# Performance work log

Measured on AMD Instinct MI355X. Metric: run time of the kernel, lower is better.

The kernel has to match this reference:

```python
import jax, jax.numpy as jnp
import numpy as np

B, S, D = 1, 2048, 1024
NH, NKV, WS = 8, 2, 64
HD = D // NH  # 128
E, HDIM, TOPK = 16, 512, 2
FP16_MIN = -65504.0
EPS = 1e-6
AUX_COEFF = 1e-5


def rmsnorm(x, w):
    return x * jax.lax.rsqrt(jnp.mean(x * x, axis=-1, keepdims=True) + EPS) * w


def setup_inputs() -> dict:
    key = jax.random.key(0)
    ks = jax.random.split(key, 24)
    r = lambda k, shape, fan: jax.random.normal(k, shape, dtype=jnp.float32) * (1.0 / np.sqrt(fan))
    return {
        "x": jax.random.normal(ks[0], (B, S, D), dtype=jnp.float32),
        "norm1_w": jnp.ones((D,), jnp.float32),
        "wq": r(ks[1], (D, NH * HD), D), "bq": jnp.zeros((NH * HD,), jnp.float32),
        "wk": r(ks[2], (D, NKV * HD), D), "bk": jnp.zeros((NKV * HD,), jnp.float32),
        "wv": r(ks[3], (D, NKV * HD), D), "bv": jnp.zeros((NKV * HD,), jnp.float32),
        "wo": r(ks[4], (NH * HD, D), NH * HD), "bo": jnp.zeros((D,), jnp.float32),
        "sink_bias": jnp.zeros((), jnp.float32),
        "norm2_w": jnp.ones((D,), jnp.float32),
        "router_w": r(ks[5], (D, E), D), "router_b": jnp.zeros((E,), jnp.float32),
        "w1": r(ks[6], (E, D, HDIM), D), "b1": jnp.zeros((E, HDIM), jnp.float32),
        "w2": r(ks[7], (E, HDIM, D), HDIM), "b2": jnp.zeros((E, D), jnp.float32),
    }


def reference(x, norm1_w, wq, bq, wk, bk, wv, bv, wo, bo, sink_bias,
              norm2_w, router_w, router_b, w1, b1, w2, b2):
    # ---- sliding-window attention with sink softmax ----
    h = rmsnorm(x, norm1_w)
    q = (h @ wq + bq).reshape(B, S, NH, HD).transpose(0, 2, 1, 3)    # [B,NH,S,HD]
    k = (h @ wk + bk).reshape(B, S, NKV, HD).transpose(0, 2, 1, 3)   # [B,NKV,S,HD]
    v = (h @ wv + bv).reshape(B, S, NKV, HD).transpose(0, 2, 1, 3)
    k = jnp.repeat(k, NH // NKV, axis=1)  # GQA expand -> [B,NH,S,HD]
    v = jnp.repeat(v, NH // NKV, axis=1)
    scores = jnp.einsum('bhqd,bhkd->bhqk', q, k) / np.sqrt(HD)
    i = jnp.arange(S)[:, None]
    j = jnp.arange(S)[None, :]
    band = (i - j >= 0) & (i - j <= WS - 1)  # causal sliding window
    scores = jnp.where(band, scores, FP16_MIN)
    m = jnp.maximum(jnp.max(scores, axis=-1, keepdims=True), sink_bias)
    ew = jnp.exp(scores - m)
    denom = jnp.sum(ew, axis=-1, keepdims=True) + jnp.exp(sink_bias - m)
    attn = ew / denom
    out = jnp.einsum('bhqk,bhkd->bhqd', attn, v).transpose(0, 2, 1, 3).reshape(B, S, D)
    x = x + (out @ wo + bo)

    # ---- MoE FFN ----
    h2 = rmsnorm(x, norm2_w)
    xf = h2.reshape(-1, D)                                  # [N,D]
    logits = (xf @ router_w + router_b) / 0.1               # [N,E]
    top_v, top_i = jax.lax.top_k(logits, TOPK)              # [N,k]
    top_w = jax.nn.softmax(top_v, axis=-1)
    probs = jax.nn.softmax(logits, axis=-1)
    aux_loss = jnp.sum(jnp.sum(probs, axis=0) ** 2) / E * AUX_COEFF
    # combine weights per (token, expert)
    gate = jnp.sum(jax.nn.one_hot(top_i, E, dtype=xf.dtype) * top_w[..., None], axis=1)  # [N,E]
    hmid = jax.nn.silu(jnp.einsum('nd,edh->neh', xf, w1) + b1)   # [N,E,H]
    y = jnp.einsum('neh,ehd->ned', hmid, w2) + b2                # [N,E,D]
    ffn = jnp.einsum('ne,ned->nd', gate, y)
    x = x + ffn.reshape(B, S, D)
    return x, aux_loss
```

## Files before the change

kernel.cpp:

```cpp
#include <hip/hip_runtime.h>
#include <hip/hip_bf16.h>

#define S     2048
#define D     1024
#define NH    8
#define NKV   2
#define HD    128
#define WS_   64
#define E_    16
#define HDIM  512
#define TOPK  2
#define NTOK  S
#define NSLOT (S*TOPK)
#define QKV_M (D + 2*NKV*HD)
#define KOFF  D
#define VOFF  (D + NKV*HD)
#define QB    4
#define WROWS (QB + WS_ - 1)
#define KPITCH 69
#define NTILES 80
#define EPAD  4096

typedef __attribute__((ext_vector_type(8))) short bf16x8;
typedef __attribute__((ext_vector_type(4))) float floatx4;

__device__ inline short f2bf(float f) {
    __hip_bfloat16 b = __float2bfloat16(f);
    return *reinterpret_cast<short*>(&b);
}

__global__ __launch_bounds__(256) void tconv_all(
    const float* __restrict__ wq, const float* __restrict__ wk,
    const float* __restrict__ wv, const float* __restrict__ wo,
    const float* __restrict__ w1, const float* __restrict__ w2,
    const float* __restrict__ bq, const float* __restrict__ bk,
    const float* __restrict__ bv, const float* __restrict__ router_w,
    short* __restrict__ wqkvT, short* __restrict__ woT,
    short* __restrict__ w1T, short* __restrict__ w2T,
    float* __restrict__ bqkv, float* __restrict__ rwT,
    const float* __restrict__ x, const float* __restrict__ norm1_w,
    short* __restrict__ h_bf, int* __restrict__ ecur)
{
    int id = blockIdx.x;
    if (id >= 9511) {
        int row = id - 9511, t = threadIdx.x;
        float4 v = ((const float4*)(x + (size_t)row * D))[t];
        float ss = v.x*v.x + v.y*v.y + v.z*v.z + v.w*v.w;
        #pragma unroll
        for (int off = 32; off; off >>= 1) ss += __shfl_xor(ss, off, 64);
        __shared__ float red[4];
        if ((t & 63) == 0) red[t >> 6] = ss;
        __syncthreads();
        float total = red[0] + red[1] + red[2] + red[3];
        float scale = rsqrtf(total * (1.0f / (float)D) + 1e-6f);
        float4 wv4 = ((const float4*)norm1_w)[t];
        short4 ob;
        ob.x = f2bf(v.x * scale * wv4.x); ob.y = f2bf(v.y * scale * wv4.y);
        ob.z = f2bf(v.z * scale * wv4.z); ob.w = f2bf(v.w * scale * wv4.w);
        ((short4*)(h_bf + (size_t)row * D))[t] = ob;
        return;
    }
    if (id == 9510) {
        int t = threadIdx.x;
        ecur[t] = 0; ecur[t + 256] = 0;
        return;
    }
    if (id >= 9478) {
        int ky = id - 9478;
        int t = threadIdx.x;
        int r = t >> 4, c = t & 15;
        int k0 = ky * 32;
        int k1 = k0 + r, k2 = k0 + r + 16;
        rwT[((k1 >> 2) << 6) + (c << 2) + (k1 & 3)] = router_w[k1 * E_ + c];
        rwT[((k2 >> 2) << 6) + (c << 2) + (k2 & 3)] = router_w[k2 * E_ + c];
        return;
    }
    if (id >= 9472) {
        int t = (id - 9472) * 256 + threadIdx.x;
        if (t < D) bqkv[t] = bq[t];
        else if (t < VOFF) bqkv[t] = bk[t - D];
        else bqkv[t] = bv[t - VOFF];
        return;
    }
    const float* in; short* outp; int K, M, mx, ky;
    if (id < 512)       { in = wq; outp = wqkvT;                  K = D; M = D;   int l = id;        mx = l & 31; ky = l >> 5; }
    else if (id < 640)  { in = wk; outp = wqkvT + (size_t)KOFF*D; K = D; M = 256; int l = id - 512;  mx = l & 7;  ky = l >> 3; }
    else if (id < 768)  { in = wv; outp = wqkvT + (size_t)VOFF*D; K = D; M = 256; int l = id - 640;  mx = l & 7;  ky = l >> 3; }
    else if (id < 1280) { in = wo; outp = woT;                    K = D; M = D;   int l = id - 768;  mx = l & 31; ky = l >> 5; }
    else if (id < 5376) { int l = id - 1280; int e = l >> 8; int r = l & 255;
                          in = w1 + (size_t)e * D * HDIM; outp = w1T + (size_t)e * D * HDIM;
                          K = D; M = HDIM; mx = r & 15; ky = r >> 4; }
    else                { int l = id - 5376; int e = l >> 8; int r = l & 255;
                          in = w2 + (size_t)e * D * HDIM; outp = w2T + (size_t)e * D * HDIM;
                          K = HDIM; M = D; mx = r & 31; ky = r >> 5; }
    __shared__ float tile[64][33];
    int t = threadIdx.x;
    int k0 = ky * 64, m0 = mx * 32;
    {
        int r = t >> 3, c4 = (t & 7) * 4;
        float4 v0 = *(const float4*)&in[(size_t)(k0 + r) * M + m0 + c4];
        float4 v1 = *(const float4*)&in[(size_t)(k0 + r + 32) * M + m0 + c4];
        tile[r][c4 + 0] = v0.x; tile[r][c4 + 1] = v0.y;
        tile[r][c4 + 2] = v0.z; tile[r][c4 + 3] = v0.w;
        tile[r + 32][c4 + 0] = v1.x; tile[r + 32][c4 + 1] = v1.y;
        tile[r + 32][c4 + 2] = v1.z; tile[r + 32][c4 + 3] = v1.w;
    }
    __syncthreads();
    {
        int mr = t >> 4, kc4 = (t & 15) * 4;
        short4 o0, o1;
        o0.x = f2bf(tile[kc4 + 0][mr]);      o0.y = f2bf(tile[kc4 + 1][mr]);
        o0.z = f2bf(tile[kc4 + 2][mr]);      o0.w = f2bf(tile[kc4 + 3][mr]);
        o1.x = f2bf(tile[kc4 + 0][mr + 16]); o1.y = f2bf(tile[kc4 + 1][mr + 16]);
        o1.z = f2bf(tile[kc4 + 2][mr + 16]); o1.w = f2bf(tile[kc4 + 3][mr + 16]);
        *(short4*)&outp[(size_t)(m0 + mr) * K + k0 + kc4] = o0;
        *(short4*)&outp[(size_t)(m0 + mr + 16) * K + k0 + kc4] = o1;
    }
}

#define BT   64
#define BKS  64
#define BUFS (BT * BKS)

__device__ inline void gld16(const short* g, short* l) {
    __builtin_amdgcn_global_load_lds(
        (const __attribute__((address_space(1))) unsigned int*)g,
        (__attribute__((address_space(3))) unsigned int*)l, 16, 0, 0);
}

template <int V>
__global__ __launch_bounds__(256) void mgemm(
    const short* __restrict__ A, const short* __restrict__ Bt,
    const float* __restrict__ bias, float* __restrict__ C,
    short* __restrict__ Cb, const float* __restrict__ res, int K, int M,
    const int* __restrict__ offs, const float* __restrict__ gatepad,
    const int* __restrict__ tokpad, const int* __restrict__ tmap)
{
    int e, row_lo, row_hi, off_e, bx;
    if (V >= 2) {
        int y = blockIdx.y;
        if (y >= tmap[NTILES]) return;
        int tm = tmap[y];
        e      = tm >> 16;
        row_lo = tm & 0xFFFF;
        off_e  = offs[e];
        row_hi = offs[e + 1];
        if (row_lo >= row_hi) return;
        bx = blockIdx.x;
    } else {
        e = 0; off_e = 0;
        int flat = blockIdx.y * gridDim.x + blockIdx.x;
        int cpx  = (gridDim.x * gridDim.y) >> 3;
        int swz  = (flat & 7) * cpx + (flat >> 3);
        bx = swz % gridDim.x;
        row_lo = (swz / gridDim.x) * BT;
        row_hi = 1 << 30;
    }
    const short* Bte = (V >= 2) ? Bt + (size_t)e * M * K : Bt;
    const float* be  = (V >= 2) ? bias + (size_t)e * M : bias;
    int col0 = bx * BT;

    __shared__ __align__(16) short As[3 * BUFS];
    __shared__ __align__(16) short Bs[3 * BUFS];

    int t = threadIdx.x;
    int wave = t >> 6, lane = t & 63;
    int lrow   = lane >> 3;
    int schunk = (lane & 7) ^ lrow;

    const short* aQ[2];
    const short* bQ[2];
    #pragma unroll
    for (int q = 0; q < 2; ++q) {
        int row = q * 32 + wave * 8 + lrow;
        int gr = row_lo + row;
        if (V >= 2 && gr >= row_hi) gr = row_lo;
        const short* arow;
        if (V == 2)
            arow = A + (size_t)(tokpad[(e << 12) + ((gr - off_e) & (EPAD - 1))]
                                & (NTOK - 1)) * K;
        else
            arow = A + (size_t)gr * K;
        aQ[q] = arow + (schunk << 3);
        bQ[q] = Bte + (size_t)(col0 + row) * K + (schunk << 3);
    }

    int rin = lane & 15, quad = lane >> 4;
    int wm = (wave & 1) * 32, wn = (wave >> 1) * 32;

    int cg0 = col0 + wn + rin;
    int cg1 = cg0 + 16;
    float bj[2] = { be[cg0], be[cg1] };
    float resv[2][2][4];
    if (V == 1) {
        #pragma unroll
        for (int i = 0; i < 2; ++i)
            #pragma unroll
            for (int j = 0; j < 2; ++j)
                #pragma unroll
                for (int rr = 0; rr < 4; ++rr)
                    resv[i][j][rr] = res[(size_t)(row_lo + wm + i*16 + quad*4 + rr) * M
                                         + (j ? cg1 : cg0)];
    }
    int   tmv[2][4];
    float tgv[2][4];
    if (V == 3) {
        #pragma unroll
        for (int i = 0; i < 2; ++i)
            #pragma unroll
            for (int rr = 0; rr < 4; ++rr) {
                int rg = row_lo + wm + i*16 + quad*4 + rr;
                int local = (rg - off_e) & (EPAD - 1);
                tmv[i][rr] = tokpad[(e << 12) + local] & (NTOK - 1);
                tgv[i][rr] = gatepad[(e << 12) + local];
            }
    }

    floatx4 acc[2][2];
    #pragma unroll
    for (int i = 0; i < 2; ++i)
        #pragma unroll
        for (int j = 0; j < 2; ++j)
            acc[i][j] = (floatx4){0.f, 0.f, 0.f, 0.f};

    const int NIT = K >> 6;

    #pragma unroll
    for (int q = 0; q < 2; ++q) {
        gld16(aQ[q], &As[(q * 32 + wave * 8) * BKS]);
        gld16(bQ[q], &Bs[(q * 32 + wave * 8) * BKS]);
    }
    if (NIT > 1) {
        #pragma unroll
        for (int q = 0; q < 2; ++q) {
            gld16(aQ[q] + 64, &As[BUFS + (q * 32 + wave * 8) * BKS]);
            gld16(bQ[q] + 64, &Bs[BUFS + (q * 32 + wave * 8) * BKS]);
        }
        asm volatile("s_waitcnt vmcnt(4)\n\ts_barrier" ::: "memory");
    } else {
        asm volatile("s_waitcnt vmcnt(0)\n\ts_barrier" ::: "memory");
    }
    __builtin_amdgcn_sched_barrier(0);

    int bread = 0;
    for (int it = 0; it < NIT; ++it) {
        if (it + 2 < NIT) {
            int bst = bread + 2; if (bst >= 3) bst -= 3;
            int kk = (it + 2) << 6;
            #pragma unroll
            for (int q = 0; q < 2; ++q) {
                gld16(aQ[q] + kk, &As[bst * BUFS + (q * 32 + wave * 8) * BKS]);
                gld16(bQ[q] + kk, &Bs[bst * BUFS + (q * 32 + wave * 8) * BKS]);
            }
        }
        const short* Ab = &As[bread * BUFS];
        const short* Bb = &Bs[bread * BUFS];
        #pragma unroll
        for (int s = 0; s < 2; ++s) {
            bf16x8 af[2], bfr[2];
            #pragma unroll
            for (int i = 0; i < 2; ++i) {
                int row = wm + i * 16 + rin;
                af[i] = *(const bf16x8*)&Ab[row * BKS
                        + ((((s << 2) | quad) ^ (rin & 7)) << 3)];
            }
            #pragma unroll
            for (int j = 0; j < 2; ++j) {
                int row = wn + j * 16 + rin;
                bfr[j] = *(const bf16x8*)&Bb[row * BKS
                        + ((((s << 2) | quad) ^ (rin & 7)) << 3)];
            }
            #pragma unroll
            for (int i = 0; i < 2; ++i)
                #pragma unroll
                for (int j = 0; j < 2; ++j)
                    acc[i][j] = __builtin_amdgcn_mfma_f32_16x16x32_bf16(
                        af[i], bfr[j], acc[i][j], 0, 0, 0);
        }
        if (it + 1 < NIT) {
            if (it + 2 < NIT)
                asm volatile("s_waitcnt vmcnt(4)\n\ts_barrier" ::: "memory");
            else
                asm volatile("s_waitcnt vmcnt(0)\n\ts_barrier" ::: "memory");
            __builtin_amdgcn_sched_barrier(0);
        }
        bread = bread + 1; if (bread >= 3) bread = 0;
    }

    #pragma unroll
    for (int i = 0; i < 2; ++i) {
        #pragma unroll
        for (int j = 0; j < 2; ++j) {
            int cg = j ? cg1 : cg0;
            #pragma unroll
            for (int rr = 0; rr < 4; ++rr) {
                int rg = row_lo + wm + i * 16 + quad * 4 + rr;
                float val = acc[i][j][rr];
                if (V == 0) {
                    C[(size_t)rg * M + cg] = val + bj[j];
                } else if (V == 1) {
                    C[(size_t)rg * M + cg] = val + bj[j] + resv[i][j][rr];
                } else if (V == 2) {
                    if (rg < row_hi) {
                        float vb_ = val + bj[j];
                        Cb[(size_t)rg * M + cg] = f2bf(vb_ / (1.f + __expf(-vb_)));
                    }
                } else {
                    if (rg < row_hi)
                        unsafeAtomicAdd(&C[(size_t)tmv[i][rr] * M + cg],
                                        tgv[i][rr] * (val + bj[j]));
                }
            }
        }
    }
}

__global__ __launch_bounds__(256, 4) void attn_kernel(
    const float* __restrict__ qkv, const float* __restrict__ sink_ptr,
    short* __restrict__ ao)
{
    __shared__ __align__(16) float KT[32 * KPITCH * 4];
    __shared__ __align__(16) float Ps4[4][64][4];

    int qblk = blockIdx.x;
    int kvh  = blockIdx.y;
    int q0   = qblk * QB;
    int jbase = q0 - (WS_ - 1);

    int t = threadIdx.x;
    int c4 = (t & 31) * 4, c4g = t & 31;
    for (int r = t >> 5; r < WROWS; r += 8) {
        int j = jbase + r;
        float4 kv4 = make_float4(0.f, 0.f, 0.f, 0.f);
        if (j >= 0)
            kv4 = *(const float4*)(qkv + (size_t)j * QKV_M + KOFF + kvh * HD + c4);
        *(float4*)&KT[(c4g * KPITCH + r) * 4] = kv4;
    }
    __syncthreads();

    int lane = t & 63, wv = t >> 6;
    float sink = sink_ptr[0];
    const float rscale = 0.08838834764831845f;

    int qi = wv;
    int i  = q0 + qi;
    bool valid = (jbase + qi + lane) >= 0;

    float sc[4] = {0.f, 0.f, 0.f, 0.f};
    const float* qbase = qkv + (size_t)i * QKV_M + (kvh * 4) * HD;
    #pragma unroll
    for (int cc = 0; cc < 16; ++cc) {
        float4 qv[4][2];
        #pragma unroll
        for (int hh = 0; hh < 4; ++hh)
            #pragma unroll
            for (int k = 0; k < 2; ++k)
                qv[hh][k] = *(const float4*)(qbase + hh * HD + (cc * 2 + k) * 4);
        #pragma unroll
        for (int k = 0; k < 2; ++k) {
            int c = cc * 2 + k;
            float4 kx = *(const float4*)&KT[(c * KPITCH + qi + lane) * 4];
            #pragma unroll
            for (int hh = 0; hh < 4; ++hh)
                sc[hh] += qv[hh][k].x*kx.x + qv[hh][k].y*kx.y
                        + qv[hh][k].z*kx.z + qv[hh][k].w*kx.w;
        }
    }

    float pn[4];
    #pragma unroll
    for (int hh = 0; hh < 4; ++hh) {
        float s = valid ? sc[hh] * rscale : -1e30f;
        float m = s;
        #pragma unroll
        for (int off = 32; off; off >>= 1) m = fmaxf(m, __shfl_xor(m, off, 64));
        float mf = fmaxf(m, sink);
        float p  = __expf(s - mf);
        float ds = p;
        #pragma unroll
        for (int off = 32; off; off >>= 1) ds += __shfl_xor(ds, off, 64);
        pn[hh] = p / (ds + __expf(sink - mf));
    }
    *(float4*)&Ps4[wv][lane][0] = make_float4(pn[0], pn[1], pn[2], pn[3]);

    float o0=0,o1=0,o2=0,o3=0,o4=0,o5=0,o6=0,o7=0;
    const float* vb = qkv + VOFF + (size_t)kvh * HD + 2 * lane;
    #pragma unroll
    for (int jb = 0; jb < 8; ++jb) {
        float2 vv[8];
        #pragma unroll
        for (int k = 0; k < 8; ++k) {
            int rj = jbase + qi + jb * 8 + k;
            rj = rj < 0 ? 0 : rj;
            vv[k] = *(const float2*)(vb + (size_t)rj * QKV_M);
        }
        #pragma unroll
        for (int k = 0; k < 8; ++k) {
            float4 p4 = *(const float4*)&Ps4[wv][jb * 8 + k][0];
            o0 += p4.x * vv[k].x; o1 += p4.x * vv[k].y;
            o2 += p4.y * vv[k].x; o3 += p4.y * vv[k].y;
            o4 += p4.z * vv[k].x; o5 += p4.z * vv[k].y;
            o6 += p4.w * vv[k].x; o7 += p4.w * vv[k].y;
        }
    }
    short2 r0; r0.x = f2bf(o0); r0.y = f2bf(o1);
    short2 r1; r1.x = f2bf(o2); r1.y = f2bf(o3);
    short2 r2; r2.x = f2bf(o4); r2.y = f2bf(o5);
    short2 r3; r3.x = f2bf(o6); r3.y = f2bf(o7);
    ((short2*)(ao + (size_t)i * D + (kvh * 4 + 0) * HD))[lane] = r0;
    ((short2*)(ao + (size_t)i * D + (kvh * 4 + 1) * HD))[lane] = r1;
    ((short2*)(ao + (size_t)i * D + (kvh * 4 + 2) * HD))[lane] = r2;
    ((short2*)(ao + (size_t)i * D + (kvh * 4 + 3) * HD))[lane] = r3;
}

__global__ __launch_bounds__(256) void rms_router_kernel(
    const float* __restrict__ x1, const float* __restrict__ w,
    short* __restrict__ h2b, const float* __restrict__ rwT,
    const float* __restrict__ rb, float* __restrict__ pcsum,
    int* __restrict__ ecur, int* __restrict__ tokpad,
    float* __restrict__ gatepad, float* __restrict__ out)
{
    __shared__ float hl[4][D];
    __shared__ float wcs[4][E_];
    int t = threadIdx.x, wv = t >> 6, lane = t & 63;
    int tok = blockIdx.x * 4 + wv;

    const float4* xr = (const float4*)(x1 + (size_t)tok * D);
    float4*      orow = (float4*)(out + (size_t)tok * D);
    const float4* wr  = (const float4*)w;
    float4 v[4], wv4[4];
    #pragma unroll
    for (int k = 0; k < 4; ++k) v[k] = xr[lane + 64 * k];
    #pragma unroll
    for (int k = 0; k < 4; ++k) wv4[k] = wr[lane + 64 * k];
    float ss = 0.f;
    #pragma unroll
    for (int k = 0; k < 4; ++k)
        ss += v[k].x*v[k].x + v[k].y*v[k].y + v[k].z*v[k].z + v[k].w*v[k].w;
    #pragma unroll
    for (int off = 32; off; off >>= 1) ss += __shfl_xor(ss, off, 64);
    float scale = rsqrtf(ss * (1.0f / (float)D) + 1e-6f);

    float4* hl4 = (float4*)hl[wv];
    short*  hb  = h2b + (size_t)tok * D;
    #pragma unroll
    for (int k = 0; k < 4; ++k) {
        orow[lane + 64 * k] = v[k];
        float4 o;
        o.x = v[k].x * scale * wv4[k].x; o.y = v[k].y * scale * wv4[k].y;
        o.z = v[k].z * scale * wv4[k].z; o.w = v[k].w * scale * wv4[k].w;
        hl4[lane + 64 * k] = o;
        short4 ob;
        ob.x = f2bf(o.x); ob.y = f2bf(o.y); ob.z = f2bf(o.z); ob.w = f2bf(o.w);
        *(short4*)&hb[(lane + 64 * k) * 4] = ob;
    }

    int q = lane >> 4;
    const float4* rw4 = (const float4*)rwT;
    float part = 0.f;
    #pragma unroll 8
    for (int i = 0; i < 64; ++i) {
        float4 a = hl4[q + 4 * i];
        float4 b = rw4[64 * i + lane];
        part += a.x * b.x; part += a.y * b.y;
        part += a.z * b.z; part += a.w * b.w;
    }
    part += __shfl_xor(part, 16, 64);
    part += __shfl_xor(part, 32, 64);

    if (lane < E_) {
        float lv = (part + rb[lane]) * 10.0f;

        float bv = lv; int bi = lane;
        #pragma unroll
        for (int off = 8; off; off >>= 1) {
            float ov = __shfl_xor(bv, off, 16);
            int   oi = __shfl_xor(bi, off, 16);
            if (ov > bv || (ov == bv && oi < bi)) { bv = ov; bi = oi; }
        }
        float lv2 = (lane == bi) ? -3.402823e38f : lv;
        float bv2 = lv2; int bi2 = lane;
        #pragma unroll
        for (int off = 8; off; off >>= 1) {
            float ov = __shfl_xor(bv2, off, 16);
            int   oi = __shfl_xor(bi2, off, 16);
            if (ov > bv2 || (ov == bv2 && oi < bi2)) { bv2 = ov; bi2 = oi; }
        }
        float pexp = __expf(lv - bv);
        float ps = pexp;
        #pragma unroll
        for (int off = 8; off; off >>= 1) ps += __shfl_xor(ps, off, 16);
        wcs[wv][lane] = pexp / ps;
        if (lane == 0) {
            float e1 = __expf(bv2 - bv);
            float g0 = 1.f / (1.f + e1);
            float g1 = e1 * g0;
            int p0 = atomicAdd(&ecur[bi  * 32], 1) & (EPAD - 1);
            int p1 = atomicAdd(&ecur[bi2 * 32], 1) & (EPAD - 1);
            tokpad[(bi  << 12) + p0] = tok;  gatepad[(bi  << 12) + p0] = g0;
            tokpad[(bi2 << 12) + p1] = tok;  gatepad[(bi2 << 12) + p1] = g1;
        }
    }
    __syncthreads();
    if (t < E_)
        pcsum[blockIdx.x * E_ + t] = wcs[0][t] + wcs[1][t] + wcs[2][t] + wcs[3][t];
}

__global__ __launch_bounds__(256) void finalize_kernel(
    const float* __restrict__ pcsum, const int* __restrict__ ecur,
    int* __restrict__ offs, int* __restrict__ tmap,
    float* __restrict__ aux_out)
{
    __shared__ float csum[E_];
    int t = threadIdx.x;
    if (t < E_) csum[t] = 0.f;
    __syncthreads();

    float part = 0.f;
    for (int i = 0; i < (S / 4) * E_ / 256; ++i)
        part += pcsum[i * 256 + t];
    atomicAdd(&csum[t & 15], part);
    __syncthreads();

    if (t == 0) {
        int acc = 0, nt = 0;
        for (int e = 0; e < E_; ++e) {
            int h = ecur[e * 32];
            offs[e] = acc;
            for (int rb = acc; rb < acc + h; rb += BT)
                tmap[nt++] = (e << 16) | rb;
            acc += h;
        }
        offs[E_] = acc;
        tmap[NTILES] = nt;
        float s = 0.f;
        for (int e = 0; e < E_; ++e) s += csum[e] * csum[e];
        *aux_out = s / (float)E_ * 1e-5f;
    }
}

extern "C" void kernel_launch(void* const* d_in, const int* in_sizes, int n_in,
                              void* d_out, int out_size, void* d_ws, size_t ws_size,
                              hipStream_t stream)
{
    const float* x        = (const float*)d_in[0];
    const float* norm1_w  = (const float*)d_in[1];
    const float* wq       = (const float*)d_in[2];
    const float* bq       = (const float*)d_in[3];
    const float* wk       = (const float*)d_in[4];
    const float* bk       = (const float*)d_in[5];
    const float* wv       = (const float*)d_in[6];
    const float* bv       = (const float*)d_in[7];
    const float* wo       = (const float*)d_in[8];
    const float* bo       = (const float*)d_in[9];
    const float* sink     = (const float*)d_in[10];
    const float* norm2_w  = (const float*)d_in[11];
    const float* router_w = (const float*)d_in[12];
    const float* router_b = (const float*)d_in[13];
    const float* w1       = (const float*)d_in[14];
    const float* b1       = (const float*)d_in[15];
    const float* w2       = (const float*)d_in[16];
    const float* b2       = (const float*)d_in[17];
    float* out = (float*)d_out;

    char* w = (char*)d_ws;
    auto alloc = [&](size_t bytes) {
        char* p = w; w += (bytes + 255) & ~255ull; return p;
    };
    short* wqkvT = (short*)alloc((size_t)QKV_M * D * 2);
    short* woT   = (short*)alloc((size_t)D * D * 2);
    short* w1T   = (short*)alloc((size_t)E_ * HDIM * D * 2);
    short* w2T   = (short*)alloc((size_t)E_ * D * HDIM * 2);
    float* bqkv  = (float*)alloc(QKV_M * 4);
    float* rwT   = (float*)alloc((size_t)E_ * D * 4);
    short* h_bf  = (short*)alloc((size_t)S * D * 2);
    float* qkv   = (float*)alloc((size_t)S * QKV_M * 4);
    float* x1    = (float*)alloc((size_t)S * D * 4);
    short* h2b   = (short*)alloc((size_t)S * D * 2);
    float* pcsum = (float*)alloc((size_t)(S / 4) * E_ * 4);
    int*   ecur     = (int*)alloc(E_ * 32 * 4);
    int*   offs     = (int*)alloc(17 * 4);
    int*   tmap     = (int*)alloc((NTILES + 1) * 4);
    int*   tokpad   = (int*)alloc((size_t)E_ * EPAD * 4);
    float* gatepad  = (float*)alloc((size_t)E_ * EPAD * 4);
    short* ao_bf = h_bf;
    short* hmid  = (short*)qkv;

    tconv_all<<<11559, 256, 0, stream>>>(wq, wk, wv, wo, w1, w2, bq, bk, bv,
                                         router_w, wqkvT, woT, w1T, w2T,
                                         bqkv, rwT, x, norm1_w, h_bf, ecur);

    mgemm<0><<<dim3(QKV_M / BT, S / BT), 256, 0, stream>>>(
        h_bf, wqkvT, bqkv, qkv, nullptr, nullptr, D, QKV_M, nullptr, nullptr,
        nullptr, nullptr);

    attn_kernel<<<dim3(S / QB, NKV), 256, 0, stream>>>(qkv, sink, ao_bf);

    mgemm<1><<<dim3(D / BT, S / BT), 256, 0, stream>>>(
        ao_bf, woT, bo, x1, nullptr, x, D, D, nullptr, nullptr, nullptr,
        nullptr);

    rms_router_kernel<<<S / 4, 256, 0, stream>>>(x1, norm2_w, h2b, rwT,
                                                 router_b, pcsum, ecur,
                                                 tokpad, gatepad, out);

    finalize_kernel<<<1, 256, 0, stream>>>(pcsum, ecur, offs, tmap,
                                           out + (size_t)S * D);

    mgemm<2><<<dim3(HDIM / BT, NTILES), 256, 0, stream>>>(
        h2b, w1T, b1, nullptr, hmid, nullptr, D, HDIM, offs, gatepad, tokpad,
        tmap);

    mgemm<3><<<dim3(D / BT, NTILES), 256, 0, stream>>>(
        hmid, w2T, b2, out, nullptr, nullptr, HDIM, D, offs, gatepad, tokpad,
        tmap);
}
```

Measured before the change: 269.9 us.

## Move expert weight transposes into the attention kernel launch

Moves the w1/w2 fp32-to-bf16 transpose blocks out of the first prep kernel and appends them as extra blocks to the attention kernel launch. The attention grid is flattened to 1D, and the shared memory is unioned between the two roles. The goal is to shorten the serial prep kernel on the critical path and let the bandwidth-bound weight conversion fill the GPU while the small attention grid runs. The risk is that the transpose blocks now inherit the attention kernel's launch bounds and shared memory size, and may slow the attention blocks through contention.

```diff
diff --git a/kernel.cpp b/kernel.cpp
--- a/kernel.cpp
+++ b/kernel.cpp
@@ -32,18 +32,16 @@
 __global__ __launch_bounds__(256) void tconv_all(
     const float* __restrict__ wq, const float* __restrict__ wk,
     const float* __restrict__ wv, const float* __restrict__ wo,
-    const float* __restrict__ w1, const float* __restrict__ w2,
     const float* __restrict__ bq, const float* __restrict__ bk,
     const float* __restrict__ bv, const float* __restrict__ router_w,
     short* __restrict__ wqkvT, short* __restrict__ woT,
-    short* __restrict__ w1T, short* __restrict__ w2T,
     float* __restrict__ bqkv, float* __restrict__ rwT,
     const float* __restrict__ x, const float* __restrict__ norm1_w,
     short* __restrict__ h_bf, int* __restrict__ ecur)
 {
     int id = blockIdx.x;
-    if (id >= 9511) {
-        int row = id - 9511, t = threadIdx.x;
+    if (id >= 1319) {
+        int row = id - 1319, t = threadIdx.x;
         float4 v = ((const float4*)(x + (size_t)row * D))[t];
         float ss = v.x*v.x + v.y*v.y + v.z*v.z + v.w*v.w;
         #pragma unroll
@@ -60,13 +58,13 @@
         ((short4*)(h_bf + (size_t)row * D))[t] = ob;
         return;
     }
-    if (id == 9510) {
+    if (id == 1318) {
         int t = threadIdx.x;
         ecur[t] = 0; ecur[t + 256] = 0;
         return;
     }
-    if (id >= 9478) {
-        int ky = id - 9478;
+    if (id >= 1286) {
+        int ky = id - 1286;
         int t = threadIdx.x;
         int r = t >> 4, c = t & 15;
         int k0 = ky * 32;
@@ -75,8 +73,8 @@
         rwT[((k2 >> 2) << 6) + (c << 2) + (k2 & 3)] = router_w[k2 * E_ + c];
         return;
     }
-    if (id >= 9472) {
-        int t = (id - 9472) * 256 + threadIdx.x;
+    if (id >= 1280) {
+        int t = (id - 1280) * 256 + threadIdx.x;
         if (t < D) bqkv[t] = bq[t];
         else if (t < VOFF) bqkv[t] = bk[t - D];
         else bqkv[t] = bv[t - VOFF];
@@ -86,13 +84,7 @@
     if (id < 512)       { in = wq; outp = wqkvT;                  K = D; M = D;   int l = id;        mx = l & 31; ky = l >> 5; }
     else if (id < 640)  { in = wk; outp = wqkvT + (size_t)KOFF*D; K = D; M = 256; int l = id - 512;  mx = l & 7;  ky = l >> 3; }
     else if (id < 768)  { in = wv; outp = wqkvT + (size_t)VOFF*D; K = D; M = 256; int l = id - 640;  mx = l & 7;  ky = l >> 3; }
-    else if (id < 1280) { in = wo; outp = woT;                    K = D; M = D;   int l = id - 768;  mx = l & 31; ky = l >> 5; }
-    else if (id < 5376) { int l = id - 1280; int e = l >> 8; int r = l & 255;
-                          in = w1 + (size_t)e * D * HDIM; outp = w1T + (size_t)e * D * HDIM;
-                          K = D; M = HDIM; mx = r & 15; ky = r >> 4; }
-    else                { int l = id - 5376; int e = l >> 8; int r = l & 255;
-                          in = w2 + (size_t)e * D * HDIM; outp = w2T + (size_t)e * D * HDIM;
-                          K = HDIM; M = D; mx = r & 31; ky = r >> 5; }
+    else                { in = wo; outp = woT;                    K = D; M = D;   int l = id - 768;  mx = l & 31; ky = l >> 5; }
     __shared__ float tile[64][33];
     int t = threadIdx.x;
     int k0 = ky * 64, m0 = mx * 32;
@@ -315,15 +307,55 @@
     }
 }
 
-__global__ __launch_bounds__(256, 4) void attn_kernel(
+__global__ __launch_bounds__(256, 4) void attn_prep_kernel(
     const float* __restrict__ qkv, const float* __restrict__ sink_ptr,
-    short* __restrict__ ao)
+    short* __restrict__ ao, const float* __restrict__ w1,
+    const float* __restrict__ w2, short* __restrict__ w1T,
+    short* __restrict__ w2T)
 {
-    __shared__ __align__(16) float KT[32 * KPITCH * 4];
-    __shared__ __align__(16) float Ps4[4][64][4];
-
-    int qblk = blockIdx.x;
-    int kvh  = blockIdx.y;
+    __shared__ __align__(16) float smem[32 * KPITCH * 4 + 4 * 64 * 4];
+
+    int bid = blockIdx.x;
+    if (bid >= 1024) {
+        int idp = bid - 1024;
+        const float* in; short* outp; int K, M, mx, ky;
+        if (idp < 4096) { int e = idp >> 8; int r = idp & 255;
+            in = w1 + (size_t)e * D * HDIM; outp = w1T + (size_t)e * D * HDIM;
+            K = D; M = HDIM; mx = r & 15; ky = r >> 4; }
+        else { int l = idp - 4096; int e = l >> 8; int r = l & 255;
+            in = w2 + (size_t)e * D * HDIM; outp = w2T + (size_t)e * D * HDIM;
+            K = HDIM; M = D; mx = r & 31; ky = r >> 5; }
+        float (*tile)[33] = (float(*)[33])smem;
+        int t = threadIdx.x;
+        int k0 = ky * 64, m0 = mx * 32;
+        {
+            int r = t >> 3, c4 = (t & 7) * 4;
+            float4 v0 = *(const float4*)&in[(size_t)(k0 + r) * M + m0 + c4];
+            float4 v1 = *(const float4*)&in[(size_t)(k0 + r + 32) * M + m0 + c4];
+            tile[r][c4 + 0] = v0.x; tile[r][c4 + 1] = v0.y;
+            tile[r][c4 + 2] = v0.z; tile[r][c4 + 3] = v0.w;
+            tile[r + 32][c4 + 0] = v1.x; tile[r + 32][c4 + 1] = v1.y;
+            tile[r + 32][c4 + 2] = v1.z; tile[r + 32][c4 + 3] = v1.w;
+        }
+        __syncthreads();
+        {
+            int mr = t >> 4, kc4 = (t & 15) * 4;
+            short4 o0, o1;
+            o0.x = f2bf(tile[kc4 + 0][mr]);      o0.y = f2bf(tile[kc4 + 1][mr]);
+            o0.z = f2bf(tile[kc4 + 2][mr]);      o0.w = f2bf(tile[kc4 + 3][mr]);
+            o1.x = f2bf(tile[kc4 + 0][mr + 16]); o1.y = f2bf(tile[kc4 + 1][mr + 16]);
+            o1.z = f2bf(tile[kc4 + 2][mr + 16]); o1.w = f2bf(tile[kc4 + 3][mr + 16]);
+            *(short4*)&outp[(size_t)(m0 + mr) * K + k0 + kc4] = o0;
+            *(short4*)&outp[(size_t)(m0 + mr + 16) * K + k0 + kc4] = o1;
+        }
+        return;
+    }
+
+    float* KT = smem;
+    float (*Ps4)[64][4] = (float(*)[64][4])(smem + 32 * KPITCH * 4);
+
+    int qblk = bid >> 1;
+    int kvh  = bid & 1;
     int q0   = qblk * QB;
     int jbase = q0 - (WS_ - 1);
 
@@ -586,15 +618,16 @@
     short* ao_bf = h_bf;
     short* hmid  = (short*)qkv;
 
-    tconv_all<<<11559, 256, 0, stream>>>(wq, wk, wv, wo, w1, w2, bq, bk, bv,
-                                         router_w, wqkvT, woT, w1T, w2T,
-                                         bqkv, rwT, x, norm1_w, h_bf, ecur);
+    tconv_all<<<3367, 256, 0, stream>>>(wq, wk, wv, wo, bq, bk, bv,
+                                        router_w, wqkvT, woT, bqkv, rwT,
+                                        x, norm1_w, h_bf, ecur);
 
     mgemm<0><<<dim3(QKV_M / BT, S / BT), 256, 0, stream>>>(
         h_bf, wqkvT, bqkv, qkv, nullptr, nullptr, D, QKV_M, nullptr, nullptr,
         nullptr, nullptr);
 
-    attn_kernel<<<dim3(S / QB, NKV), 256, 0, stream>>>(qkv, sink, ao_bf);
+    attn_prep_kernel<<<9216, 256, 0, stream>>>(qkv, sink, ao_bf,
+                                               w1, w2, w1T, w2T);
 
     mgemm<1><<<dim3(D / BT, S / BT), 256, 0, stream>>>(
         ao_bf, woT, bo, x1, nullptr, x, D, D, nullptr, nullptr, nullptr,
```

Measured after the change: 264.2 us. 1.02x faster.
